# Kernel optimization log

Hardware: AMD Instinct MI355X
Metric: run time of the kernel (lower is better)

## Reference

```python
import jax, jax.numpy as jnp
import numpy as np

V, E, U, D = 32000, 128, 256, 256
B, T = 128, 1024


def setup_inputs() -> dict:
    key = jax.random.key(0)
    k_tok, k_emb, k_wk, k_wr, k_wd = jax.random.split(key, 5)
    tokens = jax.random.randint(k_tok, (B, T), 0, V, dtype=jnp.int32)
    emb_table = jax.random.normal(k_emb, (V, E), dtype=jnp.float32) * 0.02
    Wk = jax.random.normal(k_wk, (E, 4 * U), dtype=jnp.float32) * (1.0 / np.sqrt(E))
    Wr = jax.random.normal(k_wr, (U, 4 * U), dtype=jnp.float32) * (1.0 / np.sqrt(U))
    # Keras unit_forget_bias: forget-gate bias initialized to ones (gate order i,f,g,o)
    b = jnp.concatenate([jnp.zeros((U,), jnp.float32), jnp.ones((U,), jnp.float32), jnp.zeros((2 * U,), jnp.float32)])
    Wd = jax.random.normal(k_wd, (U, D), dtype=jnp.float32) * (1.0 / np.sqrt(U))
    bd = jnp.zeros((D,), jnp.float32)
    return {"tokens": tokens, "emb_table": emb_table, "Wk": Wk, "Wr": Wr, "b": b, "Wd": Wd, "bd": bd}


def _masked_lstm(x, mask, Wk, Wr, b):
    # x: [B,T,E], mask: [B,T] bool. Keras semantics: masked steps pass
    # previous h as output and leave (h, c) unchanged.
    units = Wr.shape[0]
    bsz = x.shape[0]
    xT = jnp.swapaxes(x, 0, 1)          # [T,B,E]
    mT = jnp.swapaxes(mask, 0, 1)       # [T,B]

    def step(carry, inp):
        h, c = carry
        xt, mt = inp
        z = xt @ Wk + h @ Wr + b        # [B,4U]
        i, f, g, o = jnp.split(z, 4, axis=-1)
        i = jax.nn.sigmoid(i)
        f = jax.nn.sigmoid(f)
        g = jnp.tanh(g)
        o = jax.nn.sigmoid(o)
        c_new = f * c + i * g
        h_new = o * jnp.tanh(c_new)
        m = mt[:, None]
        h2 = jnp.where(m, h_new, h)
        c2 = jnp.where(m, c_new, c)
        return (h2, c2), h2

    h0 = jnp.zeros((bsz, units), x.dtype)
    c0 = jnp.zeros((bsz, units), x.dtype)
    _, outs = jax.lax.scan(step, (h0, c0), (xT, mT))
    return jnp.swapaxes(outs, 0, 1)     # [B,T,U]


def reference(tokens, emb_table, Wk, Wr, b, Wd, bd):
    # Embedding (mask_zero=True); dropout layers are identity at inference.
    x = emb_table[tokens]               # [B,T,E]
    mask = tokens != 0                  # [B,T]
    h = _masked_lstm(x, mask, Wk, Wr, b)  # [B,T,U]
    y = jax.nn.relu(h @ Wd + bd)        # TimeDistributed Dense(relu) -> [B,T,D]
    return y
```

## Files before the change

### kernel.cpp

```cpp
#include <hip/hip_runtime.h>
#include <cstddef>


typedef unsigned int u32x4 __attribute__((ext_vector_type(4)));

constexpr int TLEN = 1024;
constexpr int EDIM = 128;
constexpr int UDIM = 256;
constexpr int DDIM = 256;

constexpr int BPB  = 8;
constexpr int UPB  = 16;
constexpr int ZCOL = 64;
constexpr int HXROW = 432;
constexpr int ZROW = 68;

__device__ unsigned long long g_pkt[2][128][256];

__device__ __forceinline__ int pidx(int k) { return ((k >> 5) * 36) + (k & 31); }

__device__ __forceinline__ u32x4 pkt_load(const unsigned long long* p) {
  u32x4 v;
  asm volatile("global_load_dwordx4 %0, %1, off sc0 sc1" : "=v"(v) : "v"(p));
  return v;
}
#define PKT_WAIT4(a, b, c, d) \
  asm volatile("s_waitcnt vmcnt(0)" : "+v"(a), "+v"(b), "+v"(c), "+v"(d) :: "memory")

__device__ __forceinline__ float rowsum16(float v) {
  v += __int_as_float(
      __builtin_amdgcn_mov_dpp(__float_as_int(v), 0x121, 0xf, 0xf, true));
  v += __int_as_float(
      __builtin_amdgcn_mov_dpp(__float_as_int(v), 0x122, 0xf, 0xf, true));
  v += __int_as_float(
      __builtin_amdgcn_mov_dpp(__float_as_int(v), 0x124, 0xf, 0xf, true));
  v += __int_as_float(
      __builtin_amdgcn_mov_dpp(__float_as_int(v), 0x128, 0xf, 0xf, true));
  return v;
}

__global__ __launch_bounds__(256, 1) void we_lstm(
    const int* __restrict__ tokens, const float* __restrict__ emb,
    const float* __restrict__ Wk, const float* __restrict__ Wr,
    const float* __restrict__ bz, float* __restrict__ out)
{
  __shared__ float hx[2][BPB][HXROW];
  __shared__ float zs[BPB][ZROW];
  __shared__ float bias_s[ZCOL];

  const int tid = threadIdx.x;
  const int bid = blockIdx.x;
  const int bg  = bid >> 4;
  const int ug  = bid & 15;
  const int b0  = bg * BPB;
  const int u0  = ug * UPB;

  const int ksl = tid & 15;
  const int cq  = tid >> 4;

  float w[96];
#pragma unroll
  for (int i = 0; i < 6; ++i)
#pragma unroll
    for (int j = 0; j < 4; ++j) {
      const int k = ksl * 4 + i * 64 + j;
#pragma unroll
      for (int cc = 0; cc < 4; ++cc) {
        const int c   = cq * 4 + cc;
        const int col = ((c >> 4) << 8) + u0 + (c & 15);
        w[(i * 4 + j) * 4 + cc] =
            (k < UDIM) ? Wr[k * 1024 + col] : Wk[(k - UDIM) * 1024 + col];
      }
    }
  if (tid < ZCOL) bias_s[tid] = bz[((tid >> 4) << 8) + u0 + (tid & 15)];

  float creg = 0.f;
  const int gb = tid >> 4, gu = tid & 15;
  const int xb = tid >> 5, xe = (tid & 31) << 2;
  const int up = tid & 127, bq = (tid >> 7) * 4;

  float4 xv = *(const float4*)&emb[(size_t)tokens[(b0 + xb) * TLEN] * EDIM + xe];
  int tk_g = (tid < 128) ? tokens[(b0 + gb) * TLEN] : 1;

  for (int it = 0; it < TLEN; ++it) {
    const int cur = it & 1;

    *(float4*)&hx[cur][xb][pidx(UDIM + xe)] = xv;
    __syncthreads();

    float acc[8][4];
#pragma unroll
    for (int r = 0; r < 8; ++r) {
      acc[r][0] = 0.f; acc[r][1] = 0.f; acc[r][2] = 0.f; acc[r][3] = 0.f;
    }
#pragma unroll
    for (int i = 4; i < 6; ++i) {
      const int hoff = pidx(ksl * 4 + i * 64);
      float4 hv[8];
#pragma unroll
      for (int r = 0; r < 8; ++r) hv[r] = *(const float4*)&hx[cur][r][hoff];
#pragma unroll
      for (int j = 0; j < 4; ++j)
#pragma unroll
        for (int r = 0; r < 8; ++r) {
          const float hval = (j == 0) ? hv[r].x : (j == 1) ? hv[r].y
                             : (j == 2) ? hv[r].z : hv[r].w;
#pragma unroll
          for (int cc = 0; cc < 4; ++cc)
            acc[r][cc] += hval * w[(i * 4 + j) * 4 + cc];
        }
    }

    u32x4 p0, p1, p2, p3;
    const unsigned want = (unsigned)it;
    const int rp = (it + 1) & 1;
    if (it > 0) {
      p0 = pkt_load(&g_pkt[rp][b0 + bq + 0][2 * up]);
      p1 = pkt_load(&g_pkt[rp][b0 + bq + 1][2 * up]);
      p2 = pkt_load(&g_pkt[rp][b0 + bq + 2][2 * up]);
      p3 = pkt_load(&g_pkt[rp][b0 + bq + 3][2 * up]);
    }

    float4 xv_n;
    int tk_g_n = 1;
    if (it + 1 < TLEN) {
      const int tk_x = tokens[(b0 + xb) * TLEN + it + 1];
      xv_n = *(const float4*)&emb[(size_t)tk_x * EDIM + xe];
      if (tid < 128) tk_g_n = tokens[(b0 + gb) * TLEN + it + 1];
    }

    const int ho = pidx(2 * up);
    if (it > 0) {
      PKT_WAIT4(p0, p1, p2, p3);
      while (!((p0[1] == want) & (p0[3] == want) & (p1[1] == want) &
               (p1[3] == want) & (p2[1] == want) & (p2[3] == want) &
               (p3[1] == want) & (p3[3] == want))) {
        __builtin_amdgcn_s_sleep(1);
        p0 = pkt_load(&g_pkt[rp][b0 + bq + 0][2 * up]);
        p1 = pkt_load(&g_pkt[rp][b0 + bq + 1][2 * up]);
        p2 = pkt_load(&g_pkt[rp][b0 + bq + 2][2 * up]);
        p3 = pkt_load(&g_pkt[rp][b0 + bq + 3][2 * up]);
        PKT_WAIT4(p0, p1, p2, p3);
      }
      *(float2*)&hx[cur][bq + 0][ho] =
          make_float2(__uint_as_float(p0[0]), __uint_as_float(p0[2]));
      *(float2*)&hx[cur][bq + 1][ho] =
          make_float2(__uint_as_float(p1[0]), __uint_as_float(p1[2]));
      *(float2*)&hx[cur][bq + 2][ho] =
          make_float2(__uint_as_float(p2[0]), __uint_as_float(p2[2]));
      *(float2*)&hx[cur][bq + 3][ho] =
          make_float2(__uint_as_float(p3[0]), __uint_as_float(p3[2]));
    } else {
#pragma unroll
      for (int jj = 0; jj < 4; ++jj)
        *(float2*)&hx[cur][bq + jj][ho] = make_float2(0.f, 0.f);
    }
    __syncthreads();

#pragma unroll
    for (int i = 0; i < 4; ++i) {
      const int hoff = pidx(ksl * 4 + i * 64);
      float4 hv[8];
#pragma unroll
      for (int r = 0; r < 8; ++r) hv[r] = *(const float4*)&hx[cur][r][hoff];
#pragma unroll
      for (int j = 0; j < 4; ++j)
#pragma unroll
        for (int r = 0; r < 8; ++r) {
          const float hval = (j == 0) ? hv[r].x : (j == 1) ? hv[r].y
                             : (j == 2) ? hv[r].z : hv[r].w;
#pragma unroll
          for (int cc = 0; cc < 4; ++cc)
            acc[r][cc] += hval * w[(i * 4 + j) * 4 + cc];
        }
    }

#pragma unroll
    for (int r = 0; r < 8; ++r)
#pragma unroll
      for (int cc = 0; cc < 4; ++cc)
        acc[r][cc] = rowsum16(acc[r][cc]);
    if (ksl == 0) {
#pragma unroll
      for (int r = 0; r < 8; ++r)
        *(float4*)&zs[r][cq * 4] =
            make_float4(acc[r][0], acc[r][1], acc[r][2], acc[r][3]);
    }
    __syncthreads();

    if (tid < 128) {
      const float zi = zs[gb][gu]      + bias_s[gu];
      const float zf = zs[gb][16 + gu] + bias_s[16 + gu];
      const float zg = zs[gb][32 + gu] + bias_s[32 + gu];
      const float zo = zs[gb][48 + gu] + bias_s[48 + gu];
      const float gi = 1.f / (1.f + __expf(-zi));
      const float gf = 1.f / (1.f + __expf(-zf));
      const float gg = 1.f - 2.f / (1.f + __expf(2.f * zg));
      const float go = 1.f / (1.f + __expf(-zo));
      const float cn = gf * creg + gi * gg;
      const float th = 1.f - 2.f / (1.f + __expf(2.f * cn));
      const float hn = go * th;
      const bool msk = (tk_g != 0);
      const float hold = hx[cur][gb][pidx(u0 + gu)];
      const float h2 = msk ? hn : hold;
      creg = msk ? cn : creg;
      const unsigned long long pkt =
          ((unsigned long long)(unsigned)(it + 1) << 32) | __float_as_uint(h2);
      __hip_atomic_store(&g_pkt[cur][b0 + gb][u0 + gu], pkt, __ATOMIC_RELAXED,
                         __HIP_MEMORY_SCOPE_AGENT);
      __builtin_nontemporal_store(
          h2, &out[((size_t)(b0 + gb) * TLEN + it) * DDIM + u0 + gu]);
    }
    xv = xv_n;
    tk_g = tk_g_n;
  }
}

__global__ __launch_bounds__(256, 2) void we_proj(
    const float* __restrict__ Wd, const float* __restrict__ bd,
    float* __restrict__ out)
{
  __shared__ float hs[32][260];
  __shared__ float ws[32][260];
  __shared__ float bds[DDIM];

  const int tid = threadIdx.x;
  const size_t row0 = (size_t)blockIdx.x * 32;

#pragma unroll
  for (int j2 = 0; j2 < 8; ++j2) {
    const int idx = tid + j2 * 256;
    const int r = idx >> 6;
    const int cq = idx & 63;
    *(float4*)&hs[r][cq * 4] = *(const float4*)&out[(row0 + r) * DDIM + cq * 4];
  }
  bds[tid] = bd[tid];

  const int rg = tid >> 5;
  const int c0 = (tid & 31) * 8;
  float acc[4][8];
#pragma unroll
  for (int i = 0; i < 4; ++i)
#pragma unroll
    for (int c = 0; c < 8; ++c) acc[i][c] = 0.f;

  for (int kt = 0; kt < 8; ++kt) {
    __syncthreads();
#pragma unroll
    for (int j2 = 0; j2 < 8; ++j2) {
      const int idx = tid + j2 * 256;
      const int kk = idx >> 6;
      const int cq = idx & 63;
      *(float4*)&ws[kk][cq * 4] =
          *(const float4*)&Wd[(size_t)(kt * 32 + kk) * DDIM + cq * 4];
    }
    __syncthreads();
#pragma unroll
    for (int kk = 0; kk < 32; ++kk) {
      const float4 wv0 = *(const float4*)&ws[kk][c0];
      const float4 wv1 = *(const float4*)&ws[kk][c0 + 4];
#pragma unroll
      for (int i = 0; i < 4; ++i) {
        const float hval = hs[rg + i * 8][kt * 32 + kk];
        acc[i][0] += hval * wv0.x; acc[i][1] += hval * wv0.y;
        acc[i][2] += hval * wv0.z; acc[i][3] += hval * wv0.w;
        acc[i][4] += hval * wv1.x; acc[i][5] += hval * wv1.y;
        acc[i][6] += hval * wv1.z; acc[i][7] += hval * wv1.w;
      }
    }
  }
#pragma unroll
  for (int i = 0; i < 4; ++i) {
    float4 y0, y1;
    y0.x = fmaxf(acc[i][0] + bds[c0 + 0], 0.f);
    y0.y = fmaxf(acc[i][1] + bds[c0 + 1], 0.f);
    y0.z = fmaxf(acc[i][2] + bds[c0 + 2], 0.f);
    y0.w = fmaxf(acc[i][3] + bds[c0 + 3], 0.f);
    y1.x = fmaxf(acc[i][4] + bds[c0 + 4], 0.f);
    y1.y = fmaxf(acc[i][5] + bds[c0 + 5], 0.f);
    y1.z = fmaxf(acc[i][6] + bds[c0 + 6], 0.f);
    y1.w = fmaxf(acc[i][7] + bds[c0 + 7], 0.f);
    const size_t orow = (row0 + rg + i * 8) * DDIM;
    *(float4*)&out[orow + c0]     = y0;
    *(float4*)&out[orow + c0 + 4] = y1;
  }
}

extern "C" void kernel_launch(void* const* d_in, const int* in_sizes, int n_in,
                              void* d_out, int out_size, void* d_ws, size_t ws_size,
                              hipStream_t stream) {
  const int*   tokens = (const int*)d_in[0];
  const float* emb    = (const float*)d_in[1];
  const float* Wk     = (const float*)d_in[2];
  const float* Wr     = (const float*)d_in[3];
  const float* bz     = (const float*)d_in[4];
  const float* Wd     = (const float*)d_in[5];
  const float* bd     = (const float*)d_in[6];
  float* out = (float*)d_out;
  (void)in_sizes; (void)n_in; (void)out_size; (void)d_ws; (void)ws_size;
  hipLaunchKernelGGL(we_lstm, dim3(256), dim3(256), 0, stream,
                     tokens, emb, Wk, Wr, bz, out);
  hipLaunchKernelGGL(we_proj, dim3(128 * TLEN / 32), dim3(256), 0, stream,
                     Wd, bd, out);
}
```

Measured before the change: 4.104 ms.

## Remap blocks so batch groups share an XCD and poll via L2-scoped packets

Block-to-(batch group, unit group) mapping is changed so the 16 blocks exchanging h for a batch group likely land on the same XCD under round-robin dispatch. Each h packet is written twice: a workgroup-scoped copy polled with sc0 loads (L2-level) and an agent-scoped copy polled with system-coherent loads. Blocks first poll the cheaper L2 copy and permanently fall back to the coherent copy after 8 failed rounds. This aims to cut cross-die polling latency in the per-step recurrent exchange, at the cost of doubled packet stores and reliance on an assumed dispatch placement.

```diff
diff --git a/kernel.cpp b/kernel.cpp
--- a/kernel.cpp
+++ b/kernel.cpp
@@ -15,17 +15,26 @@
 constexpr int HXROW = 432;
 constexpr int ZROW = 68;
 
-__device__ unsigned long long g_pkt[2][128][256];
+__device__ unsigned long long g_pktA[2][128][256];
+__device__ unsigned long long g_pktB[2][128][256];
 
 __device__ __forceinline__ int pidx(int k) { return ((k >> 5) * 36) + (k & 31); }
 
-__device__ __forceinline__ u32x4 pkt_load(const unsigned long long* p) {
+__device__ __forceinline__ u32x4 pkt_load_ic(const unsigned long long* p) {
   u32x4 v;
   asm volatile("global_load_dwordx4 %0, %1, off sc0 sc1" : "=v"(v) : "v"(p));
   return v;
 }
+__device__ __forceinline__ u32x4 pkt_load_l2(const unsigned long long* p) {
+  u32x4 v;
+  asm volatile("global_load_dwordx4 %0, %1, off sc0" : "=v"(v) : "v"(p));
+  return v;
+}
 #define PKT_WAIT4(a, b, c, d) \
   asm volatile("s_waitcnt vmcnt(0)" : "+v"(a), "+v"(b), "+v"(c), "+v"(d) :: "memory")
+#define TAGS_OK() \
+  ((p0[1] == want) & (p0[3] == want) & (p1[1] == want) & (p1[3] == want) & \
+   (p2[1] == want) & (p2[3] == want) & (p3[1] == want) & (p3[3] == want))
 
 __device__ __forceinline__ float rowsum16(float v) {
   v += __int_as_float(
@@ -50,8 +59,8 @@
 
   const int tid = threadIdx.x;
   const int bid = blockIdx.x;
-  const int bg  = bid >> 4;
-  const int ug  = bid & 15;
+  const int bg  = ((bid & 7) << 1) | ((bid >> 3) & 1);
+  const int ug  = bid >> 4;
   const int b0  = bg * BPB;
   const int u0  = ug * UPB;
 
@@ -79,6 +88,8 @@
   const int xb = tid >> 5, xe = (tid & 31) << 2;
   const int up = tid & 127, bq = (tid >> 7) * 4;
 
+  bool use_local = true;
+
   float4 xv = *(const float4*)&emb[(size_t)tokens[(b0 + xb) * TLEN] * EDIM + xe];
   int tk_g = (tid < 128) ? tokens[(b0 + gb) * TLEN] : 1;
 
@@ -115,10 +126,17 @@
     const unsigned want = (unsigned)it;
     const int rp = (it + 1) & 1;
     if (it > 0) {
-      p0 = pkt_load(&g_pkt[rp][b0 + bq + 0][2 * up]);
-      p1 = pkt_load(&g_pkt[rp][b0 + bq + 1][2 * up]);
-      p2 = pkt_load(&g_pkt[rp][b0 + bq + 2][2 * up]);
-      p3 = pkt_load(&g_pkt[rp][b0 + bq + 3][2 * up]);
+      if (use_local) {
+        p0 = pkt_load_l2(&g_pktA[rp][b0 + bq + 0][2 * up]);
+        p1 = pkt_load_l2(&g_pktA[rp][b0 + bq + 1][2 * up]);
+        p2 = pkt_load_l2(&g_pktA[rp][b0 + bq + 2][2 * up]);
+        p3 = pkt_load_l2(&g_pktA[rp][b0 + bq + 3][2 * up]);
+      } else {
+        p0 = pkt_load_ic(&g_pktB[rp][b0 + bq + 0][2 * up]);
+        p1 = pkt_load_ic(&g_pktB[rp][b0 + bq + 1][2 * up]);
+        p2 = pkt_load_ic(&g_pktB[rp][b0 + bq + 2][2 * up]);
+        p3 = pkt_load_ic(&g_pktB[rp][b0 + bq + 3][2 * up]);
+      }
     }
 
     float4 xv_n;
@@ -132,15 +150,29 @@
     const int ho = pidx(2 * up);
     if (it > 0) {
       PKT_WAIT4(p0, p1, p2, p3);
-      while (!((p0[1] == want) & (p0[3] == want) & (p1[1] == want) &
-               (p1[3] == want) & (p2[1] == want) & (p2[3] == want) &
-               (p3[1] == want) & (p3[3] == want))) {
-        __builtin_amdgcn_s_sleep(1);
-        p0 = pkt_load(&g_pkt[rp][b0 + bq + 0][2 * up]);
-        p1 = pkt_load(&g_pkt[rp][b0 + bq + 1][2 * up]);
-        p2 = pkt_load(&g_pkt[rp][b0 + bq + 2][2 * up]);
-        p3 = pkt_load(&g_pkt[rp][b0 + bq + 3][2 * up]);
+      bool ok = TAGS_OK();
+      if (use_local) {
+        int rounds = 0;
+        while (!ok && rounds < 8) {
+          __builtin_amdgcn_s_sleep(1);
+          p0 = pkt_load_l2(&g_pktA[rp][b0 + bq + 0][2 * up]);
+          p1 = pkt_load_l2(&g_pktA[rp][b0 + bq + 1][2 * up]);
+          p2 = pkt_load_l2(&g_pktA[rp][b0 + bq + 2][2 * up]);
+          p3 = pkt_load_l2(&g_pktA[rp][b0 + bq + 3][2 * up]);
+          PKT_WAIT4(p0, p1, p2, p3);
+          ok = TAGS_OK();
+          ++rounds;
+        }
+        if (!ok) use_local = false;
+      }
+      while (!ok) {
+        p0 = pkt_load_ic(&g_pktB[rp][b0 + bq + 0][2 * up]);
+        p1 = pkt_load_ic(&g_pktB[rp][b0 + bq + 1][2 * up]);
+        p2 = pkt_load_ic(&g_pktB[rp][b0 + bq + 2][2 * up]);
+        p3 = pkt_load_ic(&g_pktB[rp][b0 + bq + 3][2 * up]);
         PKT_WAIT4(p0, p1, p2, p3);
+        ok = TAGS_OK();
+        if (!ok) __builtin_amdgcn_s_sleep(1);
       }
       *(float2*)&hx[cur][bq + 0][ho] =
           make_float2(__uint_as_float(p0[0]), __uint_as_float(p0[2]));
@@ -206,7 +238,9 @@
       creg = msk ? cn : creg;
       const unsigned long long pkt =
           ((unsigned long long)(unsigned)(it + 1) << 32) | __float_as_uint(h2);
-      __hip_atomic_store(&g_pkt[cur][b0 + gb][u0 + gu], pkt, __ATOMIC_RELAXED,
+      __hip_atomic_store(&g_pktA[cur][b0 + gb][u0 + gu], pkt, __ATOMIC_RELAXED,
+                         __HIP_MEMORY_SCOPE_WORKGROUP);
+      __hip_atomic_store(&g_pktB[cur][b0 + gb][u0 + gu], pkt, __ATOMIC_RELAXED,
                          __HIP_MEMORY_SCOPE_AGENT);
       __builtin_nontemporal_store(
           h2, &out[((size_t)(b0 + gb) * TLEN + it) * DDIM + u0 + gu]);
```

New measurement: 3.948 ms. -3.8%, faster.
